# Kernel optimization log

Hardware: AMD Instinct MI355X
Metric: run time of the kernel (lower is better)

Reference implementation:

```python
import jax, jax.numpy as jnp
import numpy as np

NUM_HEADS = 16
LN_EPS = 1e-5


def setup_inputs() -> dict:
    key = jax.random.key(0)
    ks = jax.random.split(key, 7)
    B, S, D = 4, 1024, 1024
    s_in = 1.0 / np.sqrt(D)
    return {
        "x": jax.random.normal(ks[0], (B, S, D), dtype=jnp.float32),
        # PyTorch MHA packed in-projection: [3D, D] weight, [3D] bias
        "w_qkv": jax.random.uniform(ks[1], (3 * D, D), dtype=jnp.float32, minval=-s_in, maxval=s_in),
        "b_qkv": jnp.zeros((3 * D,), dtype=jnp.float32),
        "w_out": jax.random.uniform(ks[2], (D, D), dtype=jnp.float32, minval=-s_in, maxval=s_in),
        "b_out": jnp.zeros((D,), dtype=jnp.float32),
        "ln_w": jnp.ones((D,), dtype=jnp.float32),
        "ln_b": jnp.zeros((D,), dtype=jnp.float32),
    }


def _layernorm(x, w, b):
    m = jnp.mean(x, axis=-1, keepdims=True)
    v = jnp.var(x, axis=-1, keepdims=True)
    return (x - m) * jax.lax.rsqrt(v + LN_EPS) * w + b


def reference(x, w_qkv, b_qkv, w_out, b_out, ln_w, ln_b):
    B, S, D = x.shape
    H = NUM_HEADS
    hd = D // H
    # packed QKV projection (torch: F.linear(x, w_qkv, b_qkv) then chunk)
    qkv = x @ w_qkv.T + b_qkv                      # [B, S, 3D]
    q, k, v = jnp.split(qkv, 3, axis=-1)
    q = q.reshape(B, S, H, hd).transpose(0, 2, 1, 3) * (hd ** -0.5)  # [B,H,S,hd]
    k = k.reshape(B, S, H, hd).transpose(0, 2, 1, 3)
    v = v.reshape(B, S, H, hd).transpose(0, 2, 1, 3)
    scores = jnp.einsum('bhqd,bhkd->bhqk', q, k)   # [B,H,S,S]
    attn = jax.nn.softmax(scores, axis=-1)
    ctx = jnp.einsum('bhqk,bhkd->bhqd', attn, v)   # [B,H,S,hd]
    ctx = ctx.transpose(0, 2, 1, 3).reshape(B, S, D)
    attn_out = ctx @ w_out.T + b_out
    # torch returns head-averaged weights (average_attn_weights=True)
    attn_weights = attn.mean(axis=1)               # [B,S,S]
    # dropout rate 0.0 -> identity; residual + LayerNorm
    y = _layernorm(x + attn_out, ln_w, ln_b)
    return y, attn_weights
```

## Files before the change

kernel.cpp:

```cpp
#include <hip/hip_runtime.h>
#include <cstdint>

typedef __bf16 bf16;
typedef __bf16 bf16x8 __attribute__((ext_vector_type(8)));
typedef __bf16 bf16x4 __attribute__((ext_vector_type(4)));
typedef float  f32x4  __attribute__((ext_vector_type(4)));

#define MFMA_BF16(a, b, c) __builtin_amdgcn_mfma_f32_16x16x32_bf16(a, b, c, 0, 0, 0)

#define WAITCNT_VM(n) asm volatile("s_waitcnt vmcnt(" #n ")" ::: "memory")
#define CFENCE()      asm volatile("" ::: "memory")

__device__ __forceinline__ void async_load16(const void* g, void* l) {
    __builtin_amdgcn_global_load_lds(
        (__attribute__((address_space(1))) uint32_t*)(uintptr_t)g,
        (__attribute__((address_space(3))) uint32_t*)(uint32_t)(uintptr_t)l,
        16, 0, 0);
}

__global__ void cvt_kernel(const float* __restrict__ src, bf16* __restrict__ dst, int n4) {
    int i = blockIdx.x * blockDim.x + threadIdx.x;
    if (i < n4) {
        float4 v = ((const float4*)src)[i];
        bf16x4 o;
        o[0] = (bf16)v.x; o[1] = (bf16)v.y; o[2] = (bf16)v.z; o[3] = (bf16)v.w;
        ((bf16x4*)dst)[i] = o;
    }
}

__global__ __launch_bounds__(256) void gemm_qkv_kernel(
    const bf16* __restrict__ A, const bf16* __restrict__ W,
    const float* __restrict__ bias,
    bf16* __restrict__ Qb, bf16* __restrict__ Kb, bf16* __restrict__ Vt)
{
    const int Kd = 1024;
    __shared__ bf16 sA[3][128 * 32];
    __shared__ bf16 sB[3][128 * 32];
    int tid = threadIdx.x, lane = tid & 63, wid = tid >> 6;
    int flat = blockIdx.y * 24 + blockIdx.x;
    int orig = (flat & 7) * 96 + (flat >> 3);
    int m0 = (orig / 24) * 128, n0 = (orig % 24) * 128;
    int srow = wid * 32 + (lane >> 2);
    int pchunk = lane & 3;
    int jchunk = pchunk ^ ((lane >> 3) & 3);
    const bf16* Ag = A + (size_t)(m0 + srow) * Kd + jchunk * 8;
    const bf16* Wg = W + (size_t)(n0 + srow) * Kd + jchunk * 8;
    int soff = srow * 32 + pchunk * 8;
    int wm = (wid & 1) * 64, wn = (wid >> 1) * 64;
    int lcol = lane & 15, quad = lane >> 4;
    int ckey = (lcol >> 1) & 3;
    f32x4 acc[4][4] = {};
#define STG_Q(buf, k0_) do { \
        async_load16(Ag + (k0_), &sA[buf][soff]); \
        async_load16(Ag + (k0_) + 16 * Kd, &sA[buf][soff + 512]); \
        async_load16(Wg + (k0_), &sB[buf][soff]); \
        async_load16(Wg + (k0_) + 16 * Kd, &sB[buf][soff + 512]); \
    } while (0)
    STG_Q(0, 0);
    STG_Q(1, 32);
    STG_Q(2, 64);
    int cur = 0;
    for (int it = 0; it < 32; ++it) {
        if (it < 30)      { WAITCNT_VM(8); }
        else if (it == 30){ WAITCNT_VM(4); }
        else              { WAITCNT_VM(0); }
        __builtin_amdgcn_s_barrier();
        CFENCE();
        const bf16* cA = sA[cur];
        const bf16* cB = sB[cur];
        bf16x8 af[4], bfr[4];
#pragma unroll
        for (int i = 0; i < 4; i++)
            af[i] = *(const bf16x8*)&cA[(wm + i * 16 + lcol) * 32 + (quad ^ ckey) * 8];
#pragma unroll
        for (int i = 0; i < 4; i++)
            bfr[i] = *(const bf16x8*)&cB[(wn + i * 16 + lcol) * 32 + (quad ^ ckey) * 8];
#pragma unroll
        for (int i = 0; i < 4; i++)
#pragma unroll
            for (int j = 0; j < 4; j++)
                acc[i][j] = MFMA_BF16(af[i], bfr[j], acc[i][j]);
        CFENCE();
        __builtin_amdgcn_s_barrier();
        if (it + 3 < 32) STG_Q(cur, (it + 3) * 32);
        cur = (cur == 2) ? 0 : cur + 1;
    }
#undef STG_Q
#pragma unroll
    for (int j = 0; j < 4; j++) {
        int n = n0 + wn + j * 16 + lcol;
        float bv = bias[n];
        int part = n >> 10, d = n & 1023, h = d >> 6, dd = d & 63;
#pragma unroll
        for (int i = 0; i < 4; i++) {
            int mb = m0 + wm + i * 16 + quad * 4;
            int b = mb >> 10, s = mb & 1023;
            if (part == 2) {
                bf16x4 v4;
#pragma unroll
                for (int r = 0; r < 4; r++) v4[r] = (bf16)(acc[i][j][r] + bv);
                *(bf16x4*)&Vt[(size_t)((b * 16 + h) * 64 + dd) * 1024 + s] = v4;
            } else {
                float scv = (part == 0) ? 0.125f : 1.0f;
                bf16* dst = (part == 0 ? Qb : Kb) + (size_t)((b * 16 + h) * 1024 + s) * 64 + dd;
#pragma unroll
                for (int r = 0; r < 4; r++) dst[(size_t)r * 64] = (bf16)((acc[i][j][r] + bv) * scv);
            }
        }
    }
}

__global__ __launch_bounds__(256) void gemm_out_kernel(
    const bf16* __restrict__ A, const bf16* __restrict__ W,
    const float* __restrict__ bias, float* __restrict__ out)
{
    const int Kd = 1024;
    __shared__ bf16 sA[3][64 * 32];
    __shared__ bf16 sB[3][128 * 32];
    int tid = threadIdx.x, lane = tid & 63, wid = tid >> 6;
    int m0 = blockIdx.y * 64, n0 = blockIdx.x * 128;
    int ra = tid >> 2;
    int pchunk = tid & 3;
    int jchunk = pchunk ^ ((tid >> 3) & 3);
    const bf16* Ag = A + (size_t)(m0 + ra) * Kd + jchunk * 8;
    const bf16* Wg = W + (size_t)(n0 + ra) * Kd + jchunk * 8;
    int aoff = ra * 32 + pchunk * 8;
    int wm = (wid & 1) * 32, wn = (wid >> 1) * 64;
    int lcol = lane & 15, quad = lane >> 4;
    int ckey = (lcol >> 1) & 3;
    f32x4 acc[2][4] = {};
#define STG_O(buf, k0_) do { \
        async_load16(Ag + (k0_), &sA[buf][aoff]); \
        async_load16(Wg + (k0_), &sB[buf][aoff]); \
        async_load16(Wg + (k0_) + 64 * Kd, &sB[buf][aoff + 64 * 32]); \
    } while (0)
    STG_O(0, 0);
    STG_O(1, 32);
    STG_O(2, 64);
    int cur = 0;
    for (int it = 0; it < 32; ++it) {
        if (it < 30)      { WAITCNT_VM(6); }
        else if (it == 30){ WAITCNT_VM(3); }
        else              { WAITCNT_VM(0); }
        __builtin_amdgcn_s_barrier();
        CFENCE();
        const bf16* cA = sA[cur];
        const bf16* cB = sB[cur];
        bf16x8 af[2], bfr[4];
#pragma unroll
        for (int i = 0; i < 2; i++)
            af[i] = *(const bf16x8*)&cA[(wm + i * 16 + lcol) * 32 + (quad ^ ckey) * 8];
#pragma unroll
        for (int j = 0; j < 4; j++)
            bfr[j] = *(const bf16x8*)&cB[(wn + j * 16 + lcol) * 32 + (quad ^ ckey) * 8];
#pragma unroll
        for (int i = 0; i < 2; i++)
#pragma unroll
            for (int j = 0; j < 4; j++)
                acc[i][j] = MFMA_BF16(af[i], bfr[j], acc[i][j]);
        CFENCE();
        __builtin_amdgcn_s_barrier();
        if (it + 3 < 32) STG_O(cur, (it + 3) * 32);
        cur = (cur == 2) ? 0 : cur + 1;
    }
#undef STG_O
#pragma unroll
    for (int j = 0; j < 4; j++) {
        int n = n0 + wn + j * 16 + lcol;
        float bv = bias[n];
#pragma unroll
        for (int i = 0; i < 2; i++) {
            int m = m0 + wm + i * 16 + quad * 4;
#pragma unroll
            for (int r = 0; r < 4; r++) out[(size_t)(m + r) * 1024 + n] = acc[i][j][r] + bv;
        }
    }
}

__global__ __launch_bounds__(256) void flash_kernel(
    const bf16* __restrict__ Qb, const bf16* __restrict__ Kb, const bf16* __restrict__ Vt,
    bf16* __restrict__ ctx, float* __restrict__ ml)
{
    __shared__ bf16 sK[2][64 * 64];
    __shared__ bf16 sV[2][64 * 64];
    __shared__ bf16 pt[4][16 * 64];
    int tid = threadIdx.x, lane = tid & 63, wid = tid >> 6;
    int bx = blockIdx.x;
    int orig = (bx & 7) * 128 + (bx >> 3);
    int qt = orig & 15;
    int h = (orig >> 4) & 15;
    int b = orig >> 8;
    int lcol = lane & 15, quad = lane >> 4;
    size_t base = (size_t)(b * 16 + h) * 65536;

    int q0 = qt * 64 + wid * 16;
    const bf16* qp = Qb + base + (size_t)(q0 + lcol) * 64 + quad * 8;
    bf16x8 a0 = *(const bf16x8*)qp;
    bf16x8 a1 = *(const bf16x8*)(qp + 32);

    char* wpt = (char*)&pt[wid][0];
    int rr8 = lane >> 3;
    int pp  = lane & 7;
    int jj  = pp ^ rr8;
    int sr0 = wid * 16 + rr8;
    int sw  = lcol & 7;

#define STAGE_KV(buf, kt_) do { \
        async_load16(Kb + base + (size_t)((kt_) * 64 + sr0) * 64 + jj * 8,       &sK[buf][sr0 * 64 + pp * 8]); \
        async_load16(Kb + base + (size_t)((kt_) * 64 + sr0 + 8) * 64 + jj * 8,   &sK[buf][(sr0 + 8) * 64 + pp * 8]); \
        async_load16(Vt + base + (size_t)sr0 * 1024 + (kt_) * 64 + jj * 8,       &sV[buf][sr0 * 64 + pp * 8]); \
        async_load16(Vt + base + (size_t)(sr0 + 8) * 1024 + (kt_) * 64 + jj * 8, &sV[buf][(sr0 + 8) * 64 + pp * 8]); \
    } while (0)

    float l_[4] = {0.f, 0.f, 0.f, 0.f};
    f32x4 o[4] = {};

    STAGE_KV(0, 0);
    int cur = 0;
    for (int kt = 0; kt < 16; kt++) {
        __syncthreads();
        if (kt < 15) STAGE_KV(cur ^ 1, kt + 1);
        const bf16* sKc = &sK[cur][0];
        const bf16* sVc = &sV[cur][0];
#pragma unroll
        for (int nt = 0; nt < 4; nt++) {
            int ck = quad ^ sw;
            bf16x8 bk0 = *(const bf16x8*)&sKc[(nt * 16 + lcol) * 64 + ck * 8];
            bf16x8 bk1 = *(const bf16x8*)&sKc[(nt * 16 + lcol) * 64 + (ck ^ 4) * 8];
            f32x4 s = {};
            s = MFMA_BF16(a0, bk0, s);
            s = MFMA_BF16(a1, bk1, s);
#pragma unroll
            for (int rr = 0; rr < 4; rr++) {
                float p = __expf(s[rr]);
                l_[rr] += p;
                int row = quad * 4 + rr;
                *(bf16*)(wpt + row * 128 + ((nt * 32 + lcol * 2) ^ ((row & 7) << 4))) = (bf16)p;
            }
        }
#pragma unroll
        for (int kf = 0; kf < 2; kf++) {
            bf16x8 pa = *(const bf16x8*)(wpt + lcol * 128 + (((kf * 4 + quad) ^ sw) << 4));
#pragma unroll
            for (int dt = 0; dt < 4; dt++) {
                bf16x8 vb = *(const bf16x8*)&sVc[(dt * 16 + lcol) * 64 + ((kf * 4 + quad) ^ sw) * 8];
                o[dt] = MFMA_BF16(pa, vb, o[dt]);
            }
        }
        cur ^= 1;
    }
#undef STAGE_KV
#pragma unroll
    for (int mk = 1; mk < 16; mk <<= 1)
#pragma unroll
        for (int rr = 0; rr < 4; rr++) l_[rr] += __shfl_xor(l_[rr], mk, 64);
#pragma unroll
    for (int rr = 0; rr < 4; rr++) {
        float inv = 1.f / l_[rr];
        int qg = q0 + quad * 4 + rr;
#pragma unroll
        for (int dt = 0; dt < 4; dt++)
            ctx[(size_t)(b * 1024 + qg) * 1024 + h * 64 + dt * 16 + lcol] = (bf16)(o[dt][rr] * inv);
        if (lcol == 0)
            ml[(size_t)(b * 16 + h) * 1024 + qg] = l_[rr];
    }
}

__global__ __launch_bounds__(256) void aw_kernel(
    const bf16* __restrict__ Qb, const bf16* __restrict__ Kb,
    const float* __restrict__ ml, float* __restrict__ aw)
{
    __shared__ bf16 sK[2][64 * 64];
    int tid = threadIdx.x, lane = tid & 63, wid = tid >> 6;
    int bx = blockIdx.x;
    int orig = (bx & 7) * 128 + (bx >> 3);
    int kt = orig & 15;
    int qt = (orig >> 4) & 15;
    int b = orig >> 8;
    int lcol = lane & 15, quad = lane >> 4;
    int q0 = qt * 64 + wid * 16;
    int kbase = kt * 64;
    int sw = lcol & 7;
    int r0_ = tid >> 3, p0_ = tid & 7, j0_ = p0_ ^ (r0_ & 7);
    int r1_ = (tid + 256) >> 3, p1_ = (tid + 256) & 7, j1_ = p1_ ^ (r1_ & 7);

#define STAGE_K(buf, hh) do { \
        size_t hb_ = (size_t)(b * 16 + (hh)) * 65536; \
        async_load16(Kb + hb_ + (size_t)(kbase + r0_) * 64 + j0_ * 8, &sK[buf][(size_t)tid * 8]); \
        async_load16(Kb + hb_ + (size_t)(kbase + r1_) * 64 + j1_ * 8, &sK[buf][(size_t)(tid + 256) * 8]); \
    } while (0)

    float acc[16];
#pragma unroll
    for (int i = 0; i < 16; i++) acc[i] = 0.f;

    STAGE_K(0, 0);
    int cur = 0;
    for (int h = 0; h < 16; h++) {
        size_t base = (size_t)(b * 16 + h) * 65536;
        const bf16* qp = Qb + base + (size_t)(q0 + lcol) * 64 + quad * 8;
        bf16x8 a0 = *(const bf16x8*)qp;
        bf16x8 a1 = *(const bf16x8*)(qp + 32);
        float scale[4];
#pragma unroll
        for (int rr = 0; rr < 4; rr++)
            scale[rr] = 0.0625f / ml[(size_t)(b * 16 + h) * 1024 + q0 + quad * 4 + rr];
        __syncthreads();
        if (h < 15) STAGE_K(cur ^ 1, h + 1);
#pragma unroll
        for (int nt = 0; nt < 4; nt++) {
            int ck = quad ^ sw;
            bf16x8 bk0 = *(const bf16x8*)&sK[cur][(nt * 16 + lcol) * 64 + ck * 8];
            bf16x8 bk1 = *(const bf16x8*)&sK[cur][(nt * 16 + lcol) * 64 + (ck ^ 4) * 8];
            f32x4 s = {};
            s = MFMA_BF16(a0, bk0, s);
            s = MFMA_BF16(a1, bk1, s);
#pragma unroll
            for (int rr = 0; rr < 4; rr++)
                acc[nt * 4 + rr] += __expf(s[rr]) * scale[rr];
        }
        cur ^= 1;
    }
#undef STAGE_K
#pragma unroll
    for (int nt = 0; nt < 4; nt++)
#pragma unroll
        for (int rr = 0; rr < 4; rr++)
            aw[(size_t)(b * 1024 + q0 + quad * 4 + rr) * 1024 + kbase + nt * 16 + lcol] = acc[nt * 4 + rr];
}

__global__ __launch_bounds__(256) void ln_kernel(
    const float* __restrict__ x, const float* __restrict__ ao,
    const float* __restrict__ w, const float* __restrict__ bsh,
    float* __restrict__ y)
{
    int row = blockIdx.x, tid = threadIdx.x;
    float4 xv = ((const float4*)(x + (size_t)row * 1024))[tid];
    float4 av = ((const float4*)(ao + (size_t)row * 1024))[tid];
    float4 v = {xv.x + av.x, xv.y + av.y, xv.z + av.z, xv.w + av.w};
    float s = v.x + v.y + v.z + v.w;
    float ss = v.x * v.x + v.y * v.y + v.z * v.z + v.w * v.w;
#pragma unroll
    for (int off = 32; off; off >>= 1) { s += __shfl_down(s, off); ss += __shfl_down(ss, off); }
    __shared__ float rs[4], rss[4];
    int lane = tid & 63, wid = tid >> 6;
    if (lane == 0) { rs[wid] = s; rss[wid] = ss; }
    __syncthreads();
    s = rs[0] + rs[1] + rs[2] + rs[3];
    ss = rss[0] + rss[1] + rss[2] + rss[3];
    float mean = s * (1.f / 1024.f);
    float var = ss * (1.f / 1024.f) - mean * mean;
    float inv = rsqrtf(var + 1e-5f);
    float4 wv = ((const float4*)w)[tid];
    float4 bv = ((const float4*)bsh)[tid];
    float4 o;
    o.x = (v.x - mean) * inv * wv.x + bv.x;
    o.y = (v.y - mean) * inv * wv.y + bv.y;
    o.z = (v.z - mean) * inv * wv.z + bv.z;
    o.w = (v.w - mean) * inv * wv.w + bv.w;
    ((float4*)y)[row * 256 + tid] = o;
}

extern "C" void kernel_launch(void* const* d_in, const int* in_sizes, int n_in,
                              void* d_out, int out_size, void* d_ws, size_t ws_size,
                              hipStream_t stream) {
    const float* x     = (const float*)d_in[0];
    const float* w_qkv = (const float*)d_in[1];
    const float* b_qkv = (const float*)d_in[2];
    const float* w_out = (const float*)d_in[3];
    const float* b_out = (const float*)d_in[4];
    const float* ln_w  = (const float*)d_in[5];
    const float* ln_b  = (const float*)d_in[6];

    char* ws = (char*)d_ws;
    bf16*   Qb    = (bf16*)(ws);
    bf16*   Kb    = (bf16*)(ws + (8ull  << 20));
    bf16*   Vt    = (bf16*)(ws + (16ull << 20));
    bf16*   ctx   = (bf16*)(ws + (24ull << 20));
    float*  ml    = (float*)(ws + (32ull << 20));
    bf16*   x_bf  = (bf16*)(ws + (33ull << 20));
    bf16*   wq_bf = (bf16*)(ws + (41ull << 20));
    bf16*   wo_bf = (bf16*)(ws + (16ull << 20));
    float*  ao    = (float*)(ws);

    float* y_out  = (float*)d_out;
    float* aw_out = y_out + 4ull * 1024 * 1024;

    cvt_kernel<<<4096, 256, 0, stream>>>(x, x_bf, 1048576);
    cvt_kernel<<<3072, 256, 0, stream>>>(w_qkv, wq_bf, 786432);
    gemm_qkv_kernel<<<dim3(24, 32), 256, 0, stream>>>(x_bf, wq_bf, b_qkv, Qb, Kb, Vt);
    flash_kernel<<<1024, 256, 0, stream>>>(Qb, Kb, Vt, ctx, ml);
    aw_kernel<<<1024, 256, 0, stream>>>(Qb, Kb, ml, aw_out);
    cvt_kernel<<<1024, 256, 0, stream>>>(w_out, wo_bf, 262144);
    gemm_out_kernel<<<dim3(8, 64), 256, 0, stream>>>(ctx, wo_bf, b_out, ao);
    ln_kernel<<<4096, 256, 0, stream>>>(x, ao, ln_w, ln_b, y_out);
}
```

Measured before the change: 218.1 us.

## Double flash and attn-weight query tiles to 128 rows, prefetch next-head Q in aw

The flash and attention-weight kernels now use 512-thread blocks covering 128 query rows instead of 64. Each K/V tile staged in shared memory is reused by twice as many waves, and half as many blocks are launched. The aw kernel also loads the next head's Q fragments and row sums into registers while the current head is computed, hiding global load latency. In exchange there are fewer blocks (512 on a large GPU), more shared memory per block, and more register pressure.

```diff
diff --git a/kernel.cpp b/kernel.cpp
--- a/kernel.cpp
+++ b/kernel.cpp
@@ -177,39 +177,36 @@
     }
 }
 
-__global__ __launch_bounds__(256) void flash_kernel(
+__global__ __launch_bounds__(512) void flash_kernel(
     const bf16* __restrict__ Qb, const bf16* __restrict__ Kb, const bf16* __restrict__ Vt,
     bf16* __restrict__ ctx, float* __restrict__ ml)
 {
     __shared__ bf16 sK[2][64 * 64];
     __shared__ bf16 sV[2][64 * 64];
-    __shared__ bf16 pt[4][16 * 64];
+    __shared__ bf16 pt[8][16 * 64];
     int tid = threadIdx.x, lane = tid & 63, wid = tid >> 6;
     int bx = blockIdx.x;
-    int orig = (bx & 7) * 128 + (bx >> 3);
-    int qt = orig & 15;
-    int h = (orig >> 4) & 15;
-    int b = orig >> 8;
+    int orig = (bx & 7) * 64 + (bx >> 3);
+    int qt = orig & 7;
+    int h = (orig >> 3) & 15;
+    int b = orig >> 7;
     int lcol = lane & 15, quad = lane >> 4;
     size_t base = (size_t)(b * 16 + h) * 65536;
 
-    int q0 = qt * 64 + wid * 16;
+    int q0 = qt * 128 + wid * 16;
     const bf16* qp = Qb + base + (size_t)(q0 + lcol) * 64 + quad * 8;
     bf16x8 a0 = *(const bf16x8*)qp;
     bf16x8 a1 = *(const bf16x8*)(qp + 32);
 
     char* wpt = (char*)&pt[wid][0];
-    int rr8 = lane >> 3;
-    int pp  = lane & 7;
-    int jj  = pp ^ rr8;
-    int sr0 = wid * 16 + rr8;
-    int sw  = lcol & 7;
+    int sr = tid >> 3;
+    int pp = tid & 7;
+    int jj = pp ^ (sr & 7);
+    int sw = lcol & 7;
 
 #define STAGE_KV(buf, kt_) do { \
-        async_load16(Kb + base + (size_t)((kt_) * 64 + sr0) * 64 + jj * 8,       &sK[buf][sr0 * 64 + pp * 8]); \
-        async_load16(Kb + base + (size_t)((kt_) * 64 + sr0 + 8) * 64 + jj * 8,   &sK[buf][(sr0 + 8) * 64 + pp * 8]); \
-        async_load16(Vt + base + (size_t)sr0 * 1024 + (kt_) * 64 + jj * 8,       &sV[buf][sr0 * 64 + pp * 8]); \
-        async_load16(Vt + base + (size_t)(sr0 + 8) * 1024 + (kt_) * 64 + jj * 8, &sV[buf][(sr0 + 8) * 64 + pp * 8]); \
+        async_load16(Kb + base + (size_t)((kt_) * 64 + sr) * 64 + jj * 8, &sK[buf][sr * 64 + pp * 8]); \
+        async_load16(Vt + base + (size_t)sr * 1024 + (kt_) * 64 + jj * 8, &sV[buf][sr * 64 + pp * 8]); \
     } while (0)
 
     float l_[4] = {0.f, 0.f, 0.f, 0.f};
@@ -266,59 +263,64 @@
     }
 }
 
-__global__ __launch_bounds__(256) void aw_kernel(
+__global__ __launch_bounds__(512) void aw_kernel(
     const bf16* __restrict__ Qb, const bf16* __restrict__ Kb,
     const float* __restrict__ ml, float* __restrict__ aw)
 {
     __shared__ bf16 sK[2][64 * 64];
     int tid = threadIdx.x, lane = tid & 63, wid = tid >> 6;
     int bx = blockIdx.x;
-    int orig = (bx & 7) * 128 + (bx >> 3);
+    int orig = (bx & 7) * 64 + (bx >> 3);
     int kt = orig & 15;
-    int qt = (orig >> 4) & 15;
-    int b = orig >> 8;
+    int qt = (orig >> 4) & 7;
+    int b = orig >> 7;
     int lcol = lane & 15, quad = lane >> 4;
-    int q0 = qt * 64 + wid * 16;
+    int q0 = qt * 128 + wid * 16;
     int kbase = kt * 64;
     int sw = lcol & 7;
-    int r0_ = tid >> 3, p0_ = tid & 7, j0_ = p0_ ^ (r0_ & 7);
-    int r1_ = (tid + 256) >> 3, p1_ = (tid + 256) & 7, j1_ = p1_ ^ (r1_ & 7);
-
-#define STAGE_K(buf, hh) do { \
-        size_t hb_ = (size_t)(b * 16 + (hh)) * 65536; \
-        async_load16(Kb + hb_ + (size_t)(kbase + r0_) * 64 + j0_ * 8, &sK[buf][(size_t)tid * 8]); \
-        async_load16(Kb + hb_ + (size_t)(kbase + r1_) * 64 + j1_ * 8, &sK[buf][(size_t)(tid + 256) * 8]); \
-    } while (0)
+    int sr = tid >> 3, pp = tid & 7, jj = pp ^ (sr & 7);
+
+#define STAGE_K(buf, hh) \
+        async_load16(Kb + (size_t)(b * 16 + (hh)) * 65536 + (size_t)(kbase + sr) * 64 + jj * 8, \
+                     &sK[buf][sr * 64 + pp * 8])
 
     float acc[16];
 #pragma unroll
     for (int i = 0; i < 16; i++) acc[i] = 0.f;
 
+    bf16x8 a0c, a1c, a0n, a1n;
+    float4 mvC, mvN;
+    {
+        const bf16* qp = Qb + (size_t)(b * 16) * 65536 + (size_t)(q0 + lcol) * 64 + quad * 8;
+        a0c = *(const bf16x8*)qp;
+        a1c = *(const bf16x8*)(qp + 32);
+        mvC = *(const float4*)(ml + (size_t)(b * 16) * 1024 + q0 + quad * 4);
+    }
     STAGE_K(0, 0);
     int cur = 0;
     for (int h = 0; h < 16; h++) {
-        size_t base = (size_t)(b * 16 + h) * 65536;
-        const bf16* qp = Qb + base + (size_t)(q0 + lcol) * 64 + quad * 8;
-        bf16x8 a0 = *(const bf16x8*)qp;
-        bf16x8 a1 = *(const bf16x8*)(qp + 32);
-        float scale[4];
-#pragma unroll
-        for (int rr = 0; rr < 4; rr++)
-            scale[rr] = 0.0625f / ml[(size_t)(b * 16 + h) * 1024 + q0 + quad * 4 + rr];
         __syncthreads();
-        if (h < 15) STAGE_K(cur ^ 1, h + 1);
+        if (h < 15) {
+            STAGE_K(cur ^ 1, h + 1);
+            const bf16* qp = Qb + (size_t)(b * 16 + h + 1) * 65536 + (size_t)(q0 + lcol) * 64 + quad * 8;
+            a0n = *(const bf16x8*)qp;
+            a1n = *(const bf16x8*)(qp + 32);
+            mvN = *(const float4*)(ml + (size_t)(b * 16 + h + 1) * 1024 + q0 + quad * 4);
+        }
+        float scale[4] = {0.0625f / mvC.x, 0.0625f / mvC.y, 0.0625f / mvC.z, 0.0625f / mvC.w};
 #pragma unroll
         for (int nt = 0; nt < 4; nt++) {
             int ck = quad ^ sw;
             bf16x8 bk0 = *(const bf16x8*)&sK[cur][(nt * 16 + lcol) * 64 + ck * 8];
             bf16x8 bk1 = *(const bf16x8*)&sK[cur][(nt * 16 + lcol) * 64 + (ck ^ 4) * 8];
             f32x4 s = {};
-            s = MFMA_BF16(a0, bk0, s);
-            s = MFMA_BF16(a1, bk1, s);
+            s = MFMA_BF16(a0c, bk0, s);
+            s = MFMA_BF16(a1c, bk1, s);
 #pragma unroll
             for (int rr = 0; rr < 4; rr++)
                 acc[nt * 4 + rr] += __expf(s[rr]) * scale[rr];
         }
+        if (h < 15) { a0c = a0n; a1c = a1n; mvC = mvN; }
         cur ^= 1;
     }
 #undef STAGE_K
@@ -389,8 +391,8 @@
     cvt_kernel<<<4096, 256, 0, stream>>>(x, x_bf, 1048576);
     cvt_kernel<<<3072, 256, 0, stream>>>(w_qkv, wq_bf, 786432);
     gemm_qkv_kernel<<<dim3(24, 32), 256, 0, stream>>>(x_bf, wq_bf, b_qkv, Qb, Kb, Vt);
-    flash_kernel<<<1024, 256, 0, stream>>>(Qb, Kb, Vt, ctx, ml);
-    aw_kernel<<<1024, 256, 0, stream>>>(Qb, Kb, ml, aw_out);
+    flash_kernel<<<512, 512, 0, stream>>>(Qb, Kb, Vt, ctx, ml);
+    aw_kernel<<<512, 512, 0, stream>>>(Qb, Kb, ml, aw_out);
     cvt_kernel<<<1024, 256, 0, stream>>>(w_out, wo_bf, 262144);
     gemm_out_kernel<<<dim3(8, 64), 256, 0, stream>>>(ctx, wo_bf, b_out, ao);
     ln_kernel<<<4096, 256, 0, stream>>>(x, ao, ln_w, ln_b, y_out);
```

Measured after the change: 208.9 us. 1.04x faster.
